# Kernel tuning notes

Measured on AMD Instinct MI355X. Metric: run time of the kernel, lower is better.

Reference implementation:

```python
import jax, jax.numpy as jnp
import numpy as np

E = 1024   # n_embd
H = 16     # n_heads
D = 64     # head_dim
G = 4      # n_kv_groups
F = 4096   # ffn hidden_dim
V = 32000  # vocab
L = 4      # n_layers (all full_attention)
B = 1
T = 2048
ROT = 16   # partial_rotary_factor 0.25 * head_dim 64, rounded to even
EPS = 1e-6
THETA = 10000.0


def rope_tables(seq_len):
    # matches compute_rope_params: inv_freq over even indices of rotary_dim
    inv_freq = 1.0 / (THETA ** (jnp.arange(0, ROT, 2, dtype=jnp.float32) / ROT))
    ang = jnp.arange(seq_len, dtype=jnp.float32)[:, None] * inv_freq[None, :]
    ang = jnp.concatenate([ang, ang], axis=1)  # [T, ROT]
    return jnp.cos(ang), jnp.sin(ang)


def rmsnorm(x, w):
    # torch RMSNorm: x * rsqrt(mean(x^2)+eps) * (1 + weight)
    xf = x.astype(jnp.float32)
    n = xf * jax.lax.rsqrt(jnp.mean(xf * xf, axis=-1, keepdims=True) + EPS)
    return (n * (1.0 + w)).astype(x.dtype)


def apply_rope(x, cos, sin):
    # x: [B, h, T, D]; cos/sin: [1, 1, T, ROT]; partial rotary on first ROT dims
    x_rot, x_pass = x[..., :ROT], x[..., ROT:]
    x1, x2 = x_rot[..., :ROT // 2], x_rot[..., ROT // 2:]
    rotated = jnp.concatenate([-x2, x1], axis=-1)
    return jnp.concatenate([x_rot * cos + rotated * sin, x_pass], axis=-1)


def _forward(tokens, emb, Wq, Wk, Wv, Wo, qn, kn, n1, n2, f1, f2, f3, fn, head):
    cos, sin = rope_tables(T)
    cos = cos[None, None]  # [1,1,T,ROT]
    sin = sin[None, None]
    mask = jnp.triu(jnp.ones((T, T), dtype=bool), k=1)  # True = masked
    scale = D ** -0.5
    x = emb[tokens]  # [B,T,E]

    def block(x, p):
        wq, wk, wv, wo, qw, kw, w1, w2, g1, g2, g3 = p
        h = rmsnorm(x, w1)
        # fused Q + gate projection -> [B,T,H,2D], chunk on last dim
        qg = (h @ wq).reshape(B, T, H, 2 * D)
        q = qg[..., :D].transpose(0, 2, 1, 3)            # [B,H,T,D]
        gate = qg[..., D:].reshape(B, T, H * D)          # [B,T,H*D]
        k = (h @ wk).reshape(B, T, G, D).transpose(0, 2, 1, 3)  # [B,G,T,D]
        v = (h @ wv).reshape(B, T, G, D).transpose(0, 2, 1, 3)
        q = rmsnorm(q, qw)
        k = rmsnorm(k, kw)
        q = apply_rope(q, cos, sin)
        k = apply_rope(k, cos, sin)
        k = jnp.repeat(k, H // G, axis=1)  # GQA expand -> [B,H,T,D]
        v = jnp.repeat(v, H // G, axis=1)
        scores = jnp.einsum('bhqd,bhkd->bhqk', q, k)
        scores = jnp.where(mask, -jnp.inf, scores) * scale
        w = jax.nn.softmax(scores.astype(jnp.float32), axis=-1).astype(q.dtype)
        ctx = jnp.einsum('bhqk,bhkd->bhqd', w, v)
        ctx = ctx.transpose(0, 2, 1, 3).reshape(B, T, H * D)
        ctx = ctx * jax.nn.sigmoid(gate)
        x = x + ctx @ wo
        h2 = rmsnorm(x, w2)
        ff = (jax.nn.silu(h2 @ g1) * (h2 @ g2)) @ g3
        return x + ff, None

    params = (Wq, Wk, Wv, Wo, qn, kn, n1, n2, f1, f2, f3)
    x, _ = jax.lax.scan(block, x, params)
    return rmsnorm(x, fn) @ head  # logits [B,T,V]


def setup_inputs() -> dict:
    key = jax.random.key(0)
    ks = jax.random.split(key, 16)
    s = 0.02
    rn = lambda k, shape, sc=s: jax.random.normal(k, shape, jnp.float32) * sc
    return {
        'tokens': jax.random.randint(ks[0], (B, T), 0, V),
        'emb': rn(ks[1], (V, E)),
        'Wq': rn(ks[2], (L, E, 2 * H * D)),
        'Wk': rn(ks[3], (L, E, G * D)),
        'Wv': rn(ks[4], (L, E, G * D)),
        'Wo': rn(ks[5], (L, H * D, E)),
        'qn': rn(ks[6], (L, D)),
        'kn': rn(ks[7], (L, D)),
        'n1': rn(ks[8], (L, E)),
        'n2': rn(ks[9], (L, E)),
        'f1': rn(ks[10], (L, E, F)),
        'f2': rn(ks[11], (L, E, F)),
        'f3': rn(ks[12], (L, F, E)),
        'fn': rn(ks[13], (E,)),
        'head': rn(ks[14], (E, V)),
    }


def reference(tokens, emb, Wq, Wk, Wv, Wo, qn, kn, n1, n2, f1, f2, f3, fn, head):
    return _forward(tokens, emb, Wq, Wk, Wv, Wo, qn, kn, n1, n2, f1, f2, f3, fn, head)
```

## Files before the change

kernel.cpp:

```cpp
#include <hip/hip_runtime.h>

#define T_LEN 2048
#define E_DIM 1024
#define H_N 16
#define G_N 4
#define D_H 64
#define F_DIM 4096
#define V_SZ 32000
#define L_N 4

typedef __attribute__((ext_vector_type(8))) __bf16 bf16x8;
typedef __attribute__((ext_vector_type(4))) float f32x4;

__device__ __forceinline__ unsigned short f2bf(float f){
  unsigned int u = __float_as_uint(f);
  unsigned int r = (u + 0x7FFFu + ((u >> 16) & 1u)) >> 16;
  return (unsigned short)r;
}

__device__ __forceinline__ unsigned int packbf(float a, float b){
  return (unsigned int)f2bf(a) | ((unsigned int)f2bf(b) << 16);
}

__device__ __forceinline__ f32x4 mfma16(bf16x8 a, bf16x8 b, f32x4 c){
  return __builtin_amdgcn_mfma_f32_16x16x32_bf16(a, b, c, 0, 0, 0);
}

__device__ __forceinline__ void gl16(const void* g, void* l){
  __builtin_amdgcn_global_load_lds((const __attribute__((address_space(1))) void*)g,
                                   (__attribute__((address_space(3))) void*)l, 16, 0, 0);
}

#define SBAR() __builtin_amdgcn_s_barrier()
#define LGK0() do{ asm volatile("s_waitcnt lgkmcnt(0)" ::: "memory"); __builtin_amdgcn_sched_barrier(0); }while(0)
#define VMC4() do{ asm volatile("s_waitcnt vmcnt(4)" ::: "memory"); __builtin_amdgcn_sched_barrier(0); }while(0)
#define VMC0() do{ asm volatile("s_waitcnt vmcnt(0)" ::: "memory"); __builtin_amdgcn_sched_barrier(0); }while(0)

#define QSCALE 0.1803368801111183f

__global__ __launch_bounds__(256) void embed_k(const float* __restrict__ emb,
                                               const int* __restrict__ tokens,
                                               float* __restrict__ x){
  int t = blockIdx.x;
  int tok = tokens[t];
  const float4* src = (const float4*)(emb + (size_t)tok * E_DIM);
  float4* dst = (float4*)(x + (size_t)t * E_DIM);
  dst[threadIdx.x] = src[threadIdx.x];
}

__global__ __launch_bounds__(256) void transpose_bf16(const float* __restrict__ src,
                                                      unsigned short* __restrict__ dst,
                                                      int R, int C){
  __shared__ float tile[32][33];
  int c0 = blockIdx.x * 32, r0 = blockIdx.y * 32;
  int tx = threadIdx.x & 31, ty = threadIdx.x >> 5;
  for (int i = 0; i < 4; i++){
    int r = ty + i * 8;
    tile[r][tx] = src[(size_t)(r0 + r) * C + c0 + tx];
  }
  __syncthreads();
  for (int i = 0; i < 4; i++){
    int r = ty + i * 8;
    dst[(size_t)(c0 + r) * R + r0 + tx] = f2bf(tile[tx][r]);
  }
}

__device__ __forceinline__ void tr32(const float* __restrict__ src, unsigned short* __restrict__ dst,
                                     int R, int C, int bx, int by, float* tile ){
  int c0 = bx * 32, r0 = by * 32;
  int tx = threadIdx.x & 31, ty = threadIdx.x >> 5;
  for (int i = 0; i < 4; i++){
    int r = ty + i * 8;
    tile[r * 33 + tx] = src[(size_t)(r0 + r) * C + c0 + tx];
  }
  __syncthreads();
  for (int i = 0; i < 4; i++){
    int r = ty + i * 8;
    dst[(size_t)(c0 + r) * R + r0 + tx] = f2bf(tile[tx * 33 + r]);
  }
}

__global__ __launch_bounds__(256) void prep_weights(const float* __restrict__ Wq, const float* __restrict__ Wk,
                                                    const float* __restrict__ Wv, const float* __restrict__ Wo,
                                                    const float* __restrict__ f1, const float* __restrict__ f2,
                                                    const float* __restrict__ f3,
                                                    unsigned short* __restrict__ wt_qkv,
                                                    unsigned short* __restrict__ wt_o,
                                                    unsigned short* __restrict__ wt_f12i,
                                                    unsigned short* __restrict__ wt_f3){
  __shared__ float sh[1100];
  int id = blockIdx.x;
  if (id < 2048){ tr32(Wq, wt_qkv, 1024, 2048, id & 63, id >> 6, sh); return; }
  id -= 2048;
  if (id < 256){ tr32(Wk, wt_qkv + 2048 * 1024, 1024, 256, id & 7, id >> 3, sh); return; }
  id -= 256;
  if (id < 256){ tr32(Wv, wt_qkv + 2304 * 1024, 1024, 256, id & 7, id >> 3, sh); return; }
  id -= 256;
  if (id < 1024){ tr32(Wo, wt_o, 1024, 1024, id & 31, id >> 5, sh); return; }
  id -= 1024;
  if (id < 4096){ tr32(f3, wt_f3, 4096, 1024, id & 31, id >> 5, sh); return; }
  id -= 4096;
  {
    int q = id & 255, kb = id >> 8;
    float* t1 = sh; float* t2 = sh + 32 * 17;
    int c = threadIdx.x & 15, kk0 = threadIdx.x >> 4;
    for (int p = 0; p < 2; p++){
      int kk = p * 16 + kk0;
      t1[kk * 17 + c] = f1[(size_t)(kb * 32 + kk) * F_DIM + q * 16 + c];
      t2[kk * 17 + c] = f2[(size_t)(kb * 32 + kk) * F_DIM + q * 16 + c];
    }
    __syncthreads();
    int kk = threadIdx.x & 31, rb = threadIdx.x >> 5;
    for (int i = 0; i < 4; i++){
      int r = i * 8 + rb;
      float v = (r < 16) ? t1[kk * 17 + r] : t2[kk * 17 + (r - 16)];
      wt_f12i[(size_t)(q * 32 + r) * 1024 + kb * 32 + kk] = f2bf(v);
    }
  }
}

__global__ __launch_bounds__(256) void rmsnorm_k(const float* __restrict__ x,
                                                 const float* __restrict__ w,
                                                 unsigned short* __restrict__ out){
  const int t = blockIdx.x, tid = threadIdx.x;
  const float4 v = ((const float4*)(x + (size_t)t * E_DIM))[tid];
  float ss = v.x*v.x + v.y*v.y + v.z*v.z + v.w*v.w;
  for (int m = 1; m < 64; m <<= 1) ss += __shfl_xor(ss, m);
  __shared__ float red[4];
  if ((tid & 63) == 0) red[tid >> 6] = ss;
  __syncthreads();
  ss = red[0] + red[1] + red[2] + red[3];
  const float r = rsqrtf(ss * (1.0f / E_DIM) + 1e-6f);
  const float4 wv = ((const float4*)w)[tid];
  ushort4 o;
  o.x = f2bf(v.x * r * (1.0f + wv.x));
  o.y = f2bf(v.y * r * (1.0f + wv.y));
  o.z = f2bf(v.z * r * (1.0f + wv.z));
  o.w = f2bf(v.w * r * (1.0f + wv.w));
  ((ushort4*)(out + (size_t)t * E_DIM))[tid] = o;
}

template<int MODE>
__global__ __launch_bounds__(512) void gemm128(const unsigned short* __restrict__ A,
                                               const unsigned short* __restrict__ Bt,
                                               float* __restrict__ C,
                                               int M, int N, int K){
  __shared__ unsigned short lds[49152];
  const int tid = threadIdx.x;
  const int lane = tid & 63, w = tid >> 6;
  const int wm = w >> 2, wn = w & 3;
  const int l15 = lane & 15, l4 = lane >> 4;

  const int nwg = gridDim.x;
  const int xcd = (int)blockIdx.x & 7, lin = (int)blockIdx.x >> 3;
  const int q8 = nwg >> 3, r8 = nwg & 7;
  const int wgid = (xcd < r8 ? xcd * (q8 + 1) : r8 * (q8 + 1) + (xcd - r8) * q8) + lin;
  const int nm = M >> 7;
  const int bm = wgid % nm, bn = wgid / nm;
  const int m0 = bm * 128, n0 = bn * 256;

  const int KS = K / gridDim.y;
  const int kbeg = blockIdx.y * KS;
  const int NT = KS >> 6;

  const int srow = (lane >> 3);
  const int scol = lane & 7;

  auto stageA = [&](int b, int kt){
    #pragma unroll
    for (int c = 0; c < 2; c++){
      int r = w * 16 + c * 8 + srow;
      const unsigned short* g = A + (size_t)(m0 + r) * K + kbeg + kt * 64 + ((scol ^ (r & 7)) << 3);
      gl16(g, (char*)lds + b * 16384 + (w * 16 + c * 8) * 128);
    }
  };
  auto stageB = [&](int b, int h, int kt){
    #pragma unroll
    for (int c = 0; c < 2; c++){
      int r = w * 16 + c * 8 + srow;
      const unsigned short* g = Bt + (size_t)(n0 + h * 128 + r) * K + kbeg + kt * 64 + ((scol ^ (r & 7)) << 3);
      gl16(g, (char*)lds + 32768 + (b * 2 + h) * 16384 + (w * 16 + c * 8) * 128);
    }
  };

  const int sl0 = ((l4)     ^ (l15 & 7)) << 4;
  const int sl1 = ((4 | l4) ^ (l15 & 7)) << 4;

  f32x4 acc[4][4] = {};
  bf16x8 aF[8], bF[8];

  stageA(0, 0); stageB(0, 0, 0); stageB(0, 1, 0);
  if (NT > 1){ stageB(1, 0, 1); stageB(1, 1, 1); }
  VMC4();
  SBAR();

  for (int kt = 0; kt < NT; kt++){
    const int buf = kt & 1;
    const char* Ab = (const char*)lds + buf * 16384;
    const char* Bb = (const char*)lds + 32768 + (buf * 2 + (wn >> 1)) * 16384;
    const int brbase = (wn & 1) * 64;

    #pragma unroll
    for (int mf = 0; mf < 4; mf++){
      int r = wm * 64 + mf * 16 + l15;
      aF[mf * 2 + 0] = *(const bf16x8*)(Ab + r * 128 + sl0);
      aF[mf * 2 + 1] = *(const bf16x8*)(Ab + r * 128 + sl1);
    }
    #pragma unroll
    for (int nf = 0; nf < 2; nf++){
      int r = brbase + nf * 16 + l15;
      bF[nf * 2 + 0] = *(const bf16x8*)(Bb + r * 128 + sl0);
      bF[nf * 2 + 1] = *(const bf16x8*)(Bb + r * 128 + sl1);
    }
    if (kt + 1 < NT) stageA(buf ^ 1, kt + 1);
    SBAR(); LGK0();
    __builtin_amdgcn_s_setprio(1);
    #pragma unroll
    for (int mf = 0; mf < 4; mf++)
      #pragma unroll
      for (int nf = 0; nf < 2; nf++){
        acc[mf][nf] = mfma16(aF[mf * 2 + 0], bF[nf * 2 + 0], acc[mf][nf]);
        acc[mf][nf] = mfma16(aF[mf * 2 + 1], bF[nf * 2 + 1], acc[mf][nf]);
      }
    __builtin_amdgcn_s_setprio(0);
    SBAR();

    #pragma unroll
    for (int nf = 2; nf < 4; nf++){
      int r = brbase + nf * 16 + l15;
      bF[nf * 2 + 0] = *(const bf16x8*)(Bb + r * 128 + sl0);
      bF[nf * 2 + 1] = *(const bf16x8*)(Bb + r * 128 + sl1);
    }
    SBAR(); LGK0();
    __builtin_amdgcn_s_setprio(1);
    #pragma unroll
    for (int mf = 0; mf < 4; mf++)
      #pragma unroll
      for (int nf = 2; nf < 4; nf++){
        acc[mf][nf] = mfma16(aF[mf * 2 + 0], bF[nf * 2 + 0], acc[mf][nf]);
        acc[mf][nf] = mfma16(aF[mf * 2 + 1], bF[nf * 2 + 1], acc[mf][nf]);
      }
    __builtin_amdgcn_s_setprio(0);
    SBAR();

    if (kt + 2 < NT){
      stageB(buf, 0, kt + 2);
      stageB(buf, 1, kt + 2);
      VMC4();
    } else {
      VMC0();
    }
    SBAR();
  }

  #pragma unroll
  for (int mf = 0; mf < 4; mf++)
    #pragma unroll
    for (int nf = 0; nf < 4; nf++){
      int col = n0 + wn * 64 + nf * 16 + l15;
      int row0 = m0 + wm * 64 + mf * 16 + l4 * 4;
      #pragma unroll
      for (int r = 0; r < 4; r++){
        size_t idx = (size_t)(row0 + r) * N + col;
        if (MODE == 0) C[idx] = acc[mf][nf][r];
        else atomicAdd(&C[idx], acc[mf][nf][r]);
      }
    }
}

template<int EPI>
__global__ __launch_bounds__(512, 2) void gemm256(const unsigned short* __restrict__ A,
                                                  const unsigned short* __restrict__ Bt,
                                                  float* __restrict__ outF,
                                                  unsigned short* __restrict__ outH,
                                                  int M, int N, int K){
  __shared__ unsigned short lds[65536];
  const int tid = threadIdx.x;
  const int lane = tid & 63, w = tid >> 6;
  const int wm = w >> 2, wn = w & 3;
  const int l15 = lane & 15, l4 = lane >> 4;

  const int nwg = gridDim.x;
  const int xcd = (int)blockIdx.x & 7, lin = (int)blockIdx.x >> 3;
  const int q8 = nwg >> 3, r8 = nwg & 7;
  const int wgid = (xcd < r8 ? xcd * (q8 + 1) : r8 * (q8 + 1) + (xcd - r8) * q8) + lin;
  const int nm = M >> 8;
  const int bm = wgid % nm, bn = wgid / nm;
  const int m0 = bm * 256, n0 = bn * 256;

  const int KS = K / gridDim.y;
  const int kbeg = blockIdx.y * KS;
  const int NT = KS >> 6;

  const int srow = (lane >> 3);
  const int scol = lane & 7;

  auto stageA = [&](int b, int h, int kt){
    #pragma unroll
    for (int c = 0; c < 2; c++){
      int r = w * 16 + c * 8 + srow;
      const unsigned short* g = A + (size_t)(m0 + h * 128 + r) * K + kbeg + kt * 64 + ((scol ^ (r & 7)) << 3);
      gl16(g, (char*)lds + (b * 2 + h) * 16384 + (w * 16 + c * 8) * 128);
    }
  };
  auto stageB = [&](int b, int h, int kt){
    #pragma unroll
    for (int c = 0; c < 2; c++){
      int r = w * 16 + c * 8 + srow;
      const unsigned short* g = Bt + (size_t)(n0 + h * 128 + r) * K + kbeg + kt * 64 + ((scol ^ (r & 7)) << 3);
      gl16(g, (char*)lds + 65536 + (b * 2 + h) * 16384 + (w * 16 + c * 8) * 128);
    }
  };

  const int sl0 = ((l4)     ^ (l15 & 7)) << 4;
  const int sl1 = ((4 | l4) ^ (l15 & 7)) << 4;

  f32x4 acc[8][4] = {};
  bf16x8 aF[8], bF[8];

  stageA(0, 0, 0); stageA(0, 1, 0); stageB(0, 0, 0); stageB(0, 1, 0);
  if (NT > 1){ stageB(1, 0, 1); stageB(1, 1, 1); }
  VMC4();
  SBAR();

  for (int kt = 0; kt < NT; kt++){
    const int buf = kt & 1;
    const char* Ab = (const char*)lds + (buf * 2 + wm) * 16384;
    const char* Bb = (const char*)lds + 65536 + (buf * 2 + (wn >> 1)) * 16384;
    const int brbase = (wn & 1) * 64;

    #pragma unroll
    for (int mf = 0; mf < 4; mf++){
      int r = mf * 16 + l15;
      aF[mf * 2 + 0] = *(const bf16x8*)(Ab + r * 128 + sl0);
      aF[mf * 2 + 1] = *(const bf16x8*)(Ab + r * 128 + sl1);
    }
    #pragma unroll
    for (int nf = 0; nf < 2; nf++){
      int r = brbase + nf * 16 + l15;
      bF[nf * 2 + 0] = *(const bf16x8*)(Bb + r * 128 + sl0);
      bF[nf * 2 + 1] = *(const bf16x8*)(Bb + r * 128 + sl1);
    }
    if (kt + 1 < NT) stageA(buf ^ 1, 0, kt + 1);
    SBAR(); LGK0();
    __builtin_amdgcn_s_setprio(1);
    #pragma unroll
    for (int mf = 0; mf < 4; mf++)
      #pragma unroll
      for (int nf = 0; nf < 2; nf++){
        acc[mf][nf] = mfma16(aF[mf * 2 + 0], bF[nf * 2 + 0], acc[mf][nf]);
        acc[mf][nf] = mfma16(aF[mf * 2 + 1], bF[nf * 2 + 1], acc[mf][nf]);
      }
    __builtin_amdgcn_s_setprio(0);
    SBAR();

    #pragma unroll
    for (int nf = 2; nf < 4; nf++){
      int r = brbase + nf * 16 + l15;
      bF[nf * 2 + 0] = *(const bf16x8*)(Bb + r * 128 + sl0);
      bF[nf * 2 + 1] = *(const bf16x8*)(Bb + r * 128 + sl1);
    }
    if (kt + 1 < NT) stageA(buf ^ 1, 1, kt + 1);
    SBAR(); LGK0();
    __builtin_amdgcn_s_setprio(1);
    #pragma unroll
    for (int mf = 0; mf < 4; mf++)
      #pragma unroll
      for (int nf = 2; nf < 4; nf++){
        acc[mf][nf] = mfma16(aF[mf * 2 + 0], bF[nf * 2 + 0], acc[mf][nf]);
        acc[mf][nf] = mfma16(aF[mf * 2 + 1], bF[nf * 2 + 1], acc[mf][nf]);
      }
    __builtin_amdgcn_s_setprio(0);
    SBAR();

    #pragma unroll
    for (int mf = 0; mf < 4; mf++){
      int r = 64 + mf * 16 + l15;
      aF[mf * 2 + 0] = *(const bf16x8*)(Ab + r * 128 + sl0);
      aF[mf * 2 + 1] = *(const bf16x8*)(Ab + r * 128 + sl1);
    }
    if (kt + 2 < NT) stageB(buf, 0, kt + 2);
    SBAR(); LGK0();
    __builtin_amdgcn_s_setprio(1);
    #pragma unroll
    for (int mf = 0; mf < 4; mf++)
      #pragma unroll
      for (int nf = 2; nf < 4; nf++){
        acc[4 + mf][nf] = mfma16(aF[mf * 2 + 0], bF[nf * 2 + 0], acc[4 + mf][nf]);
        acc[4 + mf][nf] = mfma16(aF[mf * 2 + 1], bF[nf * 2 + 1], acc[4 + mf][nf]);
      }
    __builtin_amdgcn_s_setprio(0);
    SBAR();

    if (kt + 2 < NT) stageB(buf, 1, kt + 2);
    SBAR();
    __builtin_amdgcn_s_setprio(1);
    #pragma unroll
    for (int mf = 0; mf < 4; mf++)
      #pragma unroll
      for (int nf = 0; nf < 2; nf++){
        acc[4 + mf][nf] = mfma16(aF[mf * 2 + 0], bF[nf * 2 + 0], acc[4 + mf][nf]);
        acc[4 + mf][nf] = mfma16(aF[mf * 2 + 1], bF[nf * 2 + 1], acc[4 + mf][nf]);
      }
    __builtin_amdgcn_s_setprio(0);
    if (kt + 2 < NT) { VMC4(); } else { VMC0(); }
    SBAR();
  }

  if (EPI == 0 || EPI == 2){
    #pragma unroll
    for (int mfg = 0; mfg < 8; mfg++){
      #pragma unroll
      for (int nf = 0; nf < 4; nf++){
        int col = n0 + wn * 64 + nf * 16 + l15;
        int row0 = m0 + wm * 128 + mfg * 16 + l4 * 4;
        #pragma unroll
        for (int r = 0; r < 4; r++){
          size_t idx = (size_t)(row0 + r) * N + col;
          if (EPI == 0) outF[idx] = acc[mfg][nf][r];
          else atomicAdd(&outF[idx], acc[mfg][nf][r]);
        }
      }
    }
  } else {
    const int NH = N >> 1;
    #pragma unroll
    for (int mfg = 0; mfg < 8; mfg++){
      #pragma unroll
      for (int nfp = 0; nfp < 2; nfp++){
        int col = (n0 >> 1) + wn * 32 + nfp * 16 + l15;
        int row0 = m0 + wm * 128 + mfg * 16 + l4 * 4;
        #pragma unroll
        for (int r = 0; r < 4; r++){
          float u = acc[mfg][nfp * 2 + 0][r];
          float g = acc[mfg][nfp * 2 + 1][r];
          outH[(size_t)(row0 + r) * NH + col] = f2bf(u / (1.0f + __expf(-u)) * g);
        }
      }
    }
  }
}

__global__ __launch_bounds__(256) void qkvpost_k(const float* __restrict__ qkv,
                                                 const float* __restrict__ qn,
                                                 const float* __restrict__ kn,
                                                 unsigned short* __restrict__ qb,
                                                 unsigned short* __restrict__ kb,
                                                 unsigned short* __restrict__ vt){
  const int t = blockIdx.x;
  const int lane = threadIdx.x & 63, w = threadIdx.x >> 6;
  const int d = lane;
  const int fi = d & 7;
  const float invf = powf(10000.0f, -(float)fi * 0.125f);
  const float ang = (float)t * invf;
  const float c = cosf(ang), s = sinf(ang);

  for (int i = 0; i < 4; i++){
    int h = w * 4 + i;
    float v = qkv[(size_t)t * 2560 + h * 128 + d];
    float ss = v * v;
    for (int m = 1; m < 64; m <<= 1) ss += __shfl_xor(ss, m);
    float r = rsqrtf(ss * (1.0f / D_H) + 1e-6f);
    float xn = v * r * (1.0f + qn[d]);
    float partner = __shfl_xor(xn, 8);
    float o;
    if (d < 8)       o = xn * c - partner * s;
    else if (d < 16) o = xn * c + partner * s;
    else             o = xn;
    qb[((size_t)h * T_LEN + t) * D_H + d] = f2bf(o * QSCALE);
  }
  {
    float v = qkv[(size_t)t * 2560 + 2048 + w * 64 + d];
    float ss = v * v;
    for (int m = 1; m < 64; m <<= 1) ss += __shfl_xor(ss, m);
    float r = rsqrtf(ss * (1.0f / D_H) + 1e-6f);
    float xn = v * r * (1.0f + kn[d]);
    float partner = __shfl_xor(xn, 8);
    float o;
    if (d < 8)       o = xn * c - partner * s;
    else if (d < 16) o = xn * c + partner * s;
    else             o = xn;
    kb[((size_t)w * T_LEN + t) * D_H + d] = f2bf(o);
  }
  {
    float v = qkv[(size_t)t * 2560 + 2304 + w * 64 + d];
    vt[((size_t)(w * 64 + d)) * T_LEN + t] = f2bf(v);
  }
}

__global__ __launch_bounds__(256) void attn_k(const unsigned short* __restrict__ qb,
                                              const unsigned short* __restrict__ kb,
                                              const unsigned short* __restrict__ vt,
                                              const float* __restrict__ qkv,
                                              unsigned short* __restrict__ ctxg){
  const int qt = blockIdx.x, h = blockIdx.y;
  const int g = h >> 2;
  const int tid = threadIdx.x;
  const int wv = tid >> 6;
  const int lane = tid & 63;
  const int l15 = lane & 15, l4 = lane >> 4;
  const int q0 = qt * 16;
  const int nch = (q0 >> 6) + 1;

  __shared__ unsigned short Pl[4][16][72];
  __shared__ float sO[4][16][66];
  __shared__ float sM[4][16];
  __shared__ float sL[4][16];

  const bf16x8 aq0 = *(const bf16x8*)(qb + ((size_t)h * T_LEN + q0 + l15) * D_H + l4 * 8);
  const bf16x8 aq1 = *(const bf16x8*)(qb + ((size_t)h * T_LEN + q0 + l15) * D_H + 32 + l4 * 8);

  f32x4 acc[4] = {};
  float m = -1e30f, lpart = 0.0f;

  for (int c = wv; c < nch; c += 4){
    const int kv0 = c << 6;
    f32x4 sc[4];
    #pragma unroll
    for (int cp = 0; cp < 4; cp++){
      const unsigned short* kbase = kb + ((size_t)g * T_LEN + kv0 + cp * 16 + l15) * D_H + l4 * 8;
      bf16x8 bk0 = *(const bf16x8*)(kbase);
      bf16x8 bk1 = *(const bf16x8*)(kbase + 32);
      f32x4 z = {0.f, 0.f, 0.f, 0.f};
      z = mfma16(bk0, aq0, z);
      z = mfma16(bk1, aq1, z);
      sc[cp] = z;
    }
    if (c == nch - 1){
      #pragma unroll
      for (int cp = 0; cp < 4; cp++)
        #pragma unroll
        for (int j = 0; j < 4; j++){
          int kv = kv0 + cp * 16 + l4 * 4 + j;
          sc[cp][j] = (kv <= q0 + l15) ? sc[cp][j] : -1e30f;
        }
    }
    float mx = sc[0][0];
    #pragma unroll
    for (int cp = 0; cp < 4; cp++)
      #pragma unroll
      for (int j = 0; j < 4; j++) mx = fmaxf(mx, sc[cp][j]);
    mx = fmaxf(mx, __shfl_xor(mx, 16));
    mx = fmaxf(mx, __shfl_xor(mx, 32));
    const float mnew = fmaxf(m, mx);
    const bool grew = !__all(mnew == m);
    const float mold = m;
    m = mnew;

    float ssum = 0.0f;
    unsigned int up[4][2];
    #pragma unroll
    for (int cp = 0; cp < 4; cp++){
      float p0 = exp2f(sc[cp][0] - mnew);
      float p1 = exp2f(sc[cp][1] - mnew);
      float p2 = exp2f(sc[cp][2] - mnew);
      float p3 = exp2f(sc[cp][3] - mnew);
      ssum += (p0 + p1) + (p2 + p3);
      up[cp][0] = packbf(p0, p1);
      up[cp][1] = packbf(p2, p3);
    }
    if (grew){
      const float resc = exp2f(mold - mnew);
      lpart *= resc;
      float r0 = __shfl(resc, l4 * 4 + 0);
      float r1 = __shfl(resc, l4 * 4 + 1);
      float r2 = __shfl(resc, l4 * 4 + 2);
      float r3 = __shfl(resc, l4 * 4 + 3);
      #pragma unroll
      for (int nt = 0; nt < 4; nt++){
        acc[nt][0] *= r0; acc[nt][1] *= r1; acc[nt][2] *= r2; acc[nt][3] *= r3;
      }
    }
    lpart += ssum;

    #pragma unroll
    for (int cp = 0; cp < 4; cp++){
      uint2 pr; pr.x = up[cp][0]; pr.y = up[cp][1];
      *(uint2*)&Pl[wv][l15][cp * 16 + l4 * 4] = pr;
    }
    asm volatile("s_waitcnt lgkmcnt(0)" ::: "memory");
    const bf16x8 pa0 = *(const bf16x8*)&Pl[wv][l15][l4 * 8];
    const bf16x8 pa1 = *(const bf16x8*)&Pl[wv][l15][32 + l4 * 8];
    #pragma unroll
    for (int nt = 0; nt < 4; nt++){
      const unsigned short* vbase = vt + ((size_t)g * 64 + nt * 16 + l15) * T_LEN + kv0;
      bf16x8 bv0 = *(const bf16x8*)(vbase + l4 * 8);
      bf16x8 bv1 = *(const bf16x8*)(vbase + 32 + l4 * 8);
      acc[nt] = mfma16(pa1, bv1, mfma16(pa0, bv0, acc[nt]));
    }
  }

  lpart += __shfl_xor(lpart, 16);
  lpart += __shfl_xor(lpart, 32);

  #pragma unroll
  for (int j = 0; j < 4; j++){
    int row = l4 * 4 + j;
    #pragma unroll
    for (int nt = 0; nt < 4; nt++)
      sO[wv][row][nt * 16 + l15] = acc[nt][j];
  }
  if (l4 == 0){
    sM[wv][l15] = m;
    sL[wv][l15] = lpart;
  }
  __syncthreads();

  #pragma unroll
  for (int rr = 0; rr < 4; rr++){
    int r = wv * 4 + rr;
    float m0 = sM[0][r], m1 = sM[1][r], m2 = sM[2][r], m3 = sM[3][r];
    float ms = fmaxf(fmaxf(m0, m1), fmaxf(m2, m3));
    float w0 = exp2f(m0 - ms), w1 = exp2f(m1 - ms), w2 = exp2f(m2 - ms), w3 = exp2f(m3 - ms);
    float accv = w0 * sO[0][r][lane] + w1 * sO[1][r][lane] + w2 * sO[2][r][lane] + w3 * sO[3][r][lane];
    float lsum = w0 * sL[0][r] + w1 * sL[1][r] + w2 * sL[2][r] + w3 * sL[3][r];
    float gate = qkv[(size_t)(q0 + r) * 2560 + h * 128 + 64 + lane];
    float val = accv / lsum * (1.0f / (1.0f + __expf(-gate)));
    ctxg[(size_t)(q0 + r) * (H_N * D_H) + h * D_H + lane] = f2bf(val);
  }
}

extern "C" void kernel_launch(void* const* d_in, const int* in_sizes, int n_in,
                              void* d_out, int out_size, void* d_ws, size_t ws_size,
                              hipStream_t stream){
  (void)in_sizes; (void)n_in; (void)out_size; (void)ws_size;
  const int*   tokens = (const int*)d_in[0];
  const float* emb    = (const float*)d_in[1];
  const float* Wq     = (const float*)d_in[2];
  const float* Wk     = (const float*)d_in[3];
  const float* Wv     = (const float*)d_in[4];
  const float* Wo     = (const float*)d_in[5];
  const float* qn     = (const float*)d_in[6];
  const float* kn     = (const float*)d_in[7];
  const float* n1     = (const float*)d_in[8];
  const float* n2     = (const float*)d_in[9];
  const float* f1     = (const float*)d_in[10];
  const float* f2     = (const float*)d_in[11];
  const float* f3     = (const float*)d_in[12];
  const float* fn     = (const float*)d_in[13];
  const float* head   = (const float*)d_in[14];
  float* out = (float*)d_out;

  char* ws = (char*)d_ws;
  size_t off = 0;
  auto alloc = [&](size_t bytes)->char*{
    char* p = ws + off;
    off += (bytes + 255) & ~(size_t)255;
    return p;
  };
  float*          x       = (float*)alloc((size_t)T_LEN * E_DIM * 4);
  unsigned short* hbf     = (unsigned short*)alloc((size_t)T_LEN * E_DIM * 2);
  float*          qkvf    = (float*)alloc((size_t)T_LEN * 2560 * 4);
  unsigned short* qb      = (unsigned short*)alloc((size_t)H_N * T_LEN * D_H * 2);
  unsigned short* kb      = (unsigned short*)alloc((size_t)G_N * T_LEN * D_H * 2);
  unsigned short* vt      = (unsigned short*)alloc((size_t)G_N * D_H * T_LEN * 2);
  unsigned short* ctxg    = (unsigned short*)alloc((size_t)T_LEN * E_DIM * 2);
  unsigned short* hg      = (unsigned short*)alloc((size_t)T_LEN * F_DIM * 2);
  unsigned short* wt_qkv  = (unsigned short*)alloc((size_t)2560 * E_DIM * 2);
  unsigned short* wt_o    = (unsigned short*)alloc((size_t)E_DIM * E_DIM * 2);
  unsigned short* wt_f12i = (unsigned short*)alloc((size_t)2 * F_DIM * E_DIM * 2);
  unsigned short* wt_f3   = (unsigned short*)alloc((size_t)E_DIM * F_DIM * 2);
  unsigned short* wt_head = (unsigned short*)alloc((size_t)V_SZ * E_DIM * 2);

  embed_k<<<T_LEN, 256, 0, stream>>>(emb, tokens, x);
  transpose_bf16<<<dim3(V_SZ / 32, E_DIM / 32), 256, 0, stream>>>(head, wt_head, E_DIM, V_SZ);

  for (int l = 0; l < L_N; l++){
    prep_weights<<<15872, 256, 0, stream>>>(Wq + (size_t)l * E_DIM * 2048,
                                            Wk + (size_t)l * E_DIM * 256,
                                            Wv + (size_t)l * E_DIM * 256,
                                            Wo + (size_t)l * E_DIM * E_DIM,
                                            f1 + (size_t)l * E_DIM * F_DIM,
                                            f2 + (size_t)l * E_DIM * F_DIM,
                                            f3 + (size_t)l * F_DIM * E_DIM,
                                            wt_qkv, wt_o, wt_f12i, wt_f3);

    rmsnorm_k<<<T_LEN, 256, 0, stream>>>(x, n1 + l * E_DIM, hbf);
    gemm128<0><<<(T_LEN / 128) * (2560 / 256), 512, 0, stream>>>(hbf, wt_qkv, qkvf, T_LEN, 2560, E_DIM);
    qkvpost_k<<<T_LEN, 256, 0, stream>>>(qkvf, qn + l * D_H, kn + l * D_H, qb, kb, vt);
    attn_k<<<dim3(T_LEN / 16, H_N), 256, 0, stream>>>(qb, kb, vt, qkvf, ctxg);
    gemm128<2><<<dim3((T_LEN / 128) * (E_DIM / 256), 4), 512, 0, stream>>>(ctxg, wt_o, x, T_LEN, E_DIM, E_DIM);

    rmsnorm_k<<<T_LEN, 256, 0, stream>>>(x, n2 + l * E_DIM, hbf);
    gemm256<1><<<(T_LEN / 256) * (2 * F_DIM / 256), 512, 0, stream>>>(hbf, wt_f12i, nullptr, hg, T_LEN, 2 * F_DIM, E_DIM);
    gemm256<2><<<dim3((T_LEN / 256) * (E_DIM / 256), 8), 512, 0, stream>>>(hg, wt_f3, x, nullptr, T_LEN, E_DIM, F_DIM);
  }

  rmsnorm_k<<<T_LEN, 256, 0, stream>>>(x, fn, hbf);
  gemm256<0><<<(T_LEN / 256) * (V_SZ / 256), 512, 0, stream>>>(hbf, wt_head, out, nullptr, T_LEN, V_SZ, E_DIM);
}
```

Before: 1.396 ms.

## Fuse QK-norm, RoPE and gate sigmoid into QKV GEMM epilogue; batch weight prep

Moves the per-head RMSNorm, partial RoPE, Q scaling, K/V layout conversion and gate sigmoid into the QKV GEMM epilogue. This removes the fp32 qkv intermediate and the separate qkvpost kernel, and attention now reads the gate as a precomputed bf16 sigmoid. Weight transposition for all layers is also launched once, ahead of the layer loop, into per-layer buffers. The cost is a larger workspace, more epilogue register pressure with cos/sin computed per element, and scattered stores for the V transpose.

```diff
diff --git a/kernel.cpp b/kernel.cpp
--- a/kernel.cpp
+++ b/kernel.cpp
@@ -16,6 +16,10 @@
   unsigned int u = __float_as_uint(f);
   unsigned int r = (u + 0x7FFFu + ((u >> 16) & 1u)) >> 16;
   return (unsigned short)r;
+}
+
+__device__ __forceinline__ float bf2f(unsigned short u){
+  return __uint_as_float((unsigned int)u << 16);
 }
 
 __device__ __forceinline__ unsigned int packbf(float a, float b){
@@ -80,16 +84,32 @@
   }
 }
 
-__global__ __launch_bounds__(256) void prep_weights(const float* __restrict__ Wq, const float* __restrict__ Wk,
-                                                    const float* __restrict__ Wv, const float* __restrict__ Wo,
-                                                    const float* __restrict__ f1, const float* __restrict__ f2,
-                                                    const float* __restrict__ f3,
-                                                    unsigned short* __restrict__ wt_qkv,
-                                                    unsigned short* __restrict__ wt_o,
-                                                    unsigned short* __restrict__ wt_f12i,
-                                                    unsigned short* __restrict__ wt_f3){
+#define PREP_PER_LAYER 15872
+
+__global__ __launch_bounds__(256) void prep_weights(const float* __restrict__ Wq_, const float* __restrict__ Wk_,
+                                                    const float* __restrict__ Wv_, const float* __restrict__ Wo_,
+                                                    const float* __restrict__ f1_, const float* __restrict__ f2_,
+                                                    const float* __restrict__ f3_,
+                                                    unsigned short* __restrict__ wt_qkv_,
+                                                    unsigned short* __restrict__ wt_o_,
+                                                    unsigned short* __restrict__ wt_f12i_,
+                                                    unsigned short* __restrict__ wt_f3_){
   __shared__ float sh[1100];
   int id = blockIdx.x;
+  const int l = id / PREP_PER_LAYER;
+  id -= l * PREP_PER_LAYER;
+  const float* Wq = Wq_ + (size_t)l * E_DIM * 2048;
+  const float* Wk = Wk_ + (size_t)l * E_DIM * 256;
+  const float* Wv = Wv_ + (size_t)l * E_DIM * 256;
+  const float* Wo = Wo_ + (size_t)l * E_DIM * E_DIM;
+  const float* f1 = f1_ + (size_t)l * E_DIM * F_DIM;
+  const float* f2 = f2_ + (size_t)l * E_DIM * F_DIM;
+  const float* f3 = f3_ + (size_t)l * F_DIM * E_DIM;
+  unsigned short* wt_qkv  = wt_qkv_  + (size_t)l * 2560 * E_DIM;
+  unsigned short* wt_o    = wt_o_    + (size_t)l * E_DIM * E_DIM;
+  unsigned short* wt_f12i = wt_f12i_ + (size_t)l * 2 * F_DIM * E_DIM;
+  unsigned short* wt_f3   = wt_f3_   + (size_t)l * E_DIM * F_DIM;
+
   if (id < 2048){ tr32(Wq, wt_qkv, 1024, 2048, id & 63, id >> 6, sh); return; }
   id -= 2048;
   if (id < 256){ tr32(Wk, wt_qkv + 2048 * 1024, 1024, 256, id & 7, id >> 3, sh); return; }
@@ -144,7 +164,13 @@
 __global__ __launch_bounds__(512) void gemm128(const unsigned short* __restrict__ A,
                                                const unsigned short* __restrict__ Bt,
                                                float* __restrict__ C,
-                                               int M, int N, int K){
+                                               int M, int N, int K,
+                                               const float* __restrict__ qn,
+                                               const float* __restrict__ kn,
+                                               unsigned short* __restrict__ qb,
+                                               unsigned short* __restrict__ kb,
+                                               unsigned short* __restrict__ vtb,
+                                               unsigned short* __restrict__ sg){
   __shared__ unsigned short lds[49152];
   const int tid = threadIdx.x;
   const int lane = tid & 63, w = tid >> 6;
@@ -253,19 +279,106 @@
     SBAR();
   }
 
-  #pragma unroll
-  for (int mf = 0; mf < 4; mf++)
-    #pragma unroll
-    for (int nf = 0; nf < 4; nf++){
-      int col = n0 + wn * 64 + nf * 16 + l15;
-      int row0 = m0 + wm * 64 + mf * 16 + l4 * 4;
-      #pragma unroll
-      for (int r = 0; r < 4; r++){
-        size_t idx = (size_t)(row0 + r) * N + col;
-        if (MODE == 0) C[idx] = acc[mf][nf][r];
-        else atomicAdd(&C[idx], acc[mf][nf][r]);
-      }
-    }
+  if (MODE == 0 || MODE == 2){
+    #pragma unroll
+    for (int mf = 0; mf < 4; mf++)
+      #pragma unroll
+      for (int nf = 0; nf < 4; nf++){
+        int col = n0 + wn * 64 + nf * 16 + l15;
+        int row0 = m0 + wm * 64 + mf * 16 + l4 * 4;
+        #pragma unroll
+        for (int r = 0; r < 4; r++){
+          size_t idx = (size_t)(row0 + r) * N + col;
+          if (MODE == 0) C[idx] = acc[mf][nf][r];
+          else atomicAdd(&C[idx], acc[mf][nf][r]);
+        }
+      }
+  } else {
+    const int cbase = n0 + wn * 64;
+    if (cbase < 2048){
+      const int h = cbase >> 7;
+      if ((cbase & 64) == 0){
+        const float qw0 = qn[l15], qw1 = qn[16 + l15], qw2 = qn[32 + l15], qw3 = qn[48 + l15];
+        const float invf = powf(10000.0f, -(float)(l15 & 7) * 0.125f);
+        #pragma unroll
+        for (int mf = 0; mf < 4; mf++)
+          #pragma unroll
+          for (int r = 0; r < 4; r++){
+            float ss = 0.0f;
+            #pragma unroll
+            for (int nf = 0; nf < 4; nf++) ss += acc[mf][nf][r] * acc[mf][nf][r];
+            ss += __shfl_xor(ss, 1); ss += __shfl_xor(ss, 2);
+            ss += __shfl_xor(ss, 4); ss += __shfl_xor(ss, 8);
+            const float rs = rsqrtf(ss * (1.0f / 64.0f) + 1e-6f);
+            const int t = m0 + wm * 64 + mf * 16 + l4 * 4 + r;
+            const float ang = (float)t * invf;
+            const float cc = cosf(ang), sn = sinf(ang);
+            float x0 = acc[mf][0][r] * rs * (1.0f + qw0);
+            float x1 = acc[mf][1][r] * rs * (1.0f + qw1);
+            float x2 = acc[mf][2][r] * rs * (1.0f + qw2);
+            float x3 = acc[mf][3][r] * rs * (1.0f + qw3);
+            float partner = __shfl_xor(x0, 8);
+            float o0 = (l15 < 8) ? (x0 * cc - partner * sn) : (x0 * cc + partner * sn);
+            unsigned short* qrow = qb + ((size_t)h * T_LEN + t) * 64;
+            qrow[l15]      = f2bf(o0 * QSCALE);
+            qrow[16 + l15] = f2bf(x1 * QSCALE);
+            qrow[32 + l15] = f2bf(x2 * QSCALE);
+            qrow[48 + l15] = f2bf(x3 * QSCALE);
+          }
+      } else {
+        #pragma unroll
+        for (int mf = 0; mf < 4; mf++)
+          #pragma unroll
+          for (int r = 0; r < 4; r++){
+            const int t = m0 + wm * 64 + mf * 16 + l4 * 4 + r;
+            unsigned short* srow = sg + (size_t)t * 1024 + h * 64;
+            #pragma unroll
+            for (int nf = 0; nf < 4; nf++)
+              srow[nf * 16 + l15] = f2bf(1.0f / (1.0f + __expf(-acc[mf][nf][r])));
+          }
+      }
+    } else if (cbase < 2304){
+      const int g = (cbase - 2048) >> 6;
+      const float kw0 = kn[l15], kw1 = kn[16 + l15], kw2 = kn[32 + l15], kw3 = kn[48 + l15];
+      const float invf = powf(10000.0f, -(float)(l15 & 7) * 0.125f);
+      #pragma unroll
+      for (int mf = 0; mf < 4; mf++)
+        #pragma unroll
+        for (int r = 0; r < 4; r++){
+          float ss = 0.0f;
+          #pragma unroll
+          for (int nf = 0; nf < 4; nf++) ss += acc[mf][nf][r] * acc[mf][nf][r];
+          ss += __shfl_xor(ss, 1); ss += __shfl_xor(ss, 2);
+          ss += __shfl_xor(ss, 4); ss += __shfl_xor(ss, 8);
+          const float rs = rsqrtf(ss * (1.0f / 64.0f) + 1e-6f);
+          const int t = m0 + wm * 64 + mf * 16 + l4 * 4 + r;
+          const float ang = (float)t * invf;
+          const float cc = cosf(ang), sn = sinf(ang);
+          float x0 = acc[mf][0][r] * rs * (1.0f + kw0);
+          float x1 = acc[mf][1][r] * rs * (1.0f + kw1);
+          float x2 = acc[mf][2][r] * rs * (1.0f + kw2);
+          float x3 = acc[mf][3][r] * rs * (1.0f + kw3);
+          float partner = __shfl_xor(x0, 8);
+          float o0 = (l15 < 8) ? (x0 * cc - partner * sn) : (x0 * cc + partner * sn);
+          unsigned short* krow = kb + ((size_t)g * T_LEN + t) * 64;
+          krow[l15]      = f2bf(o0);
+          krow[16 + l15] = f2bf(x1);
+          krow[32 + l15] = f2bf(x2);
+          krow[48 + l15] = f2bf(x3);
+        }
+    } else {
+      const int g = (cbase - 2304) >> 6;
+      #pragma unroll
+      for (int mf = 0; mf < 4; mf++)
+        #pragma unroll
+        for (int r = 0; r < 4; r++){
+          const int t = m0 + wm * 64 + mf * 16 + l4 * 4 + r;
+          #pragma unroll
+          for (int nf = 0; nf < 4; nf++)
+            vtb[((size_t)g * 64 + nf * 16 + l15) * T_LEN + t] = f2bf(acc[mf][nf][r]);
+        }
+    }
+  }
 }
 
 template<int EPI>
@@ -441,57 +554,10 @@
   }
 }
 
-__global__ __launch_bounds__(256) void qkvpost_k(const float* __restrict__ qkv,
-                                                 const float* __restrict__ qn,
-                                                 const float* __restrict__ kn,
-                                                 unsigned short* __restrict__ qb,
-                                                 unsigned short* __restrict__ kb,
-                                                 unsigned short* __restrict__ vt){
-  const int t = blockIdx.x;
-  const int lane = threadIdx.x & 63, w = threadIdx.x >> 6;
-  const int d = lane;
-  const int fi = d & 7;
-  const float invf = powf(10000.0f, -(float)fi * 0.125f);
-  const float ang = (float)t * invf;
-  const float c = cosf(ang), s = sinf(ang);
-
-  for (int i = 0; i < 4; i++){
-    int h = w * 4 + i;
-    float v = qkv[(size_t)t * 2560 + h * 128 + d];
-    float ss = v * v;
-    for (int m = 1; m < 64; m <<= 1) ss += __shfl_xor(ss, m);
-    float r = rsqrtf(ss * (1.0f / D_H) + 1e-6f);
-    float xn = v * r * (1.0f + qn[d]);
-    float partner = __shfl_xor(xn, 8);
-    float o;
-    if (d < 8)       o = xn * c - partner * s;
-    else if (d < 16) o = xn * c + partner * s;
-    else             o = xn;
-    qb[((size_t)h * T_LEN + t) * D_H + d] = f2bf(o * QSCALE);
-  }
-  {
-    float v = qkv[(size_t)t * 2560 + 2048 + w * 64 + d];
-    float ss = v * v;
-    for (int m = 1; m < 64; m <<= 1) ss += __shfl_xor(ss, m);
-    float r = rsqrtf(ss * (1.0f / D_H) + 1e-6f);
-    float xn = v * r * (1.0f + kn[d]);
-    float partner = __shfl_xor(xn, 8);
-    float o;
-    if (d < 8)       o = xn * c - partner * s;
-    else if (d < 16) o = xn * c + partner * s;
-    else             o = xn;
-    kb[((size_t)w * T_LEN + t) * D_H + d] = f2bf(o);
-  }
-  {
-    float v = qkv[(size_t)t * 2560 + 2304 + w * 64 + d];
-    vt[((size_t)(w * 64 + d)) * T_LEN + t] = f2bf(v);
-  }
-}
-
 __global__ __launch_bounds__(256) void attn_k(const unsigned short* __restrict__ qb,
                                               const unsigned short* __restrict__ kb,
                                               const unsigned short* __restrict__ vt,
-                                              const float* __restrict__ qkv,
+                                              const unsigned short* __restrict__ sgate,
                                               unsigned short* __restrict__ ctxg){
   const int qt = blockIdx.x, h = blockIdx.y;
   const int g = h >> 2;
@@ -614,8 +680,8 @@
     float w0 = exp2f(m0 - ms), w1 = exp2f(m1 - ms), w2 = exp2f(m2 - ms), w3 = exp2f(m3 - ms);
     float accv = w0 * sO[0][r][lane] + w1 * sO[1][r][lane] + w2 * sO[2][r][lane] + w3 * sO[3][r][lane];
     float lsum = w0 * sL[0][r] + w1 * sL[1][r] + w2 * sL[2][r] + w3 * sL[3][r];
-    float gate = qkv[(size_t)(q0 + r) * 2560 + h * 128 + 64 + lane];
-    float val = accv / lsum * (1.0f / (1.0f + __expf(-gate)));
+    float sgv = bf2f(sgate[(size_t)(q0 + r) * 1024 + h * 64 + lane]);
+    float val = accv / lsum * sgv;
     ctxg[(size_t)(q0 + r) * (H_N * D_H) + h * D_H + lane] = f2bf(val);
   }
 }
@@ -648,38 +714,37 @@
     off += (bytes + 255) & ~(size_t)255;
     return p;
   };
-  float*          x       = (float*)alloc((size_t)T_LEN * E_DIM * 4);
-  unsigned short* hbf     = (unsigned short*)alloc((size_t)T_LEN * E_DIM * 2);
-  float*          qkvf    = (float*)alloc((size_t)T_LEN * 2560 * 4);
-  unsigned short* qb      = (unsigned short*)alloc((size_t)H_N * T_LEN * D_H * 2);
-  unsigned short* kb      = (unsigned short*)alloc((size_t)G_N * T_LEN * D_H * 2);
-  unsigned short* vt      = (unsigned short*)alloc((size_t)G_N * D_H * T_LEN * 2);
-  unsigned short* ctxg    = (unsigned short*)alloc((size_t)T_LEN * E_DIM * 2);
-  unsigned short* hg      = (unsigned short*)alloc((size_t)T_LEN * F_DIM * 2);
-  unsigned short* wt_qkv  = (unsigned short*)alloc((size_t)2560 * E_DIM * 2);
-  unsigned short* wt_o    = (unsigned short*)alloc((size_t)E_DIM * E_DIM * 2);
-  unsigned short* wt_f12i = (unsigned short*)alloc((size_t)2 * F_DIM * E_DIM * 2);
-  unsigned short* wt_f3   = (unsigned short*)alloc((size_t)E_DIM * F_DIM * 2);
-  unsigned short* wt_head = (unsigned short*)alloc((size_t)V_SZ * E_DIM * 2);
+  float*          x        = (float*)alloc((size_t)T_LEN * E_DIM * 4);
+  unsigned short* hbf      = (unsigned short*)alloc((size_t)T_LEN * E_DIM * 2);
+  unsigned short* qb       = (unsigned short*)alloc((size_t)H_N * T_LEN * D_H * 2);
+  unsigned short* kb       = (unsigned short*)alloc((size_t)G_N * T_LEN * D_H * 2);
+  unsigned short* vt       = (unsigned short*)alloc((size_t)G_N * D_H * T_LEN * 2);
+  unsigned short* sgate    = (unsigned short*)alloc((size_t)T_LEN * E_DIM * 2);
+  unsigned short* ctxg     = (unsigned short*)alloc((size_t)T_LEN * E_DIM * 2);
+  unsigned short* hg       = (unsigned short*)alloc((size_t)T_LEN * F_DIM * 2);
+  unsigned short* wt_qkv4  = (unsigned short*)alloc((size_t)L_N * 2560 * E_DIM * 2);
+  unsigned short* wt_o4    = (unsigned short*)alloc((size_t)L_N * E_DIM * E_DIM * 2);
+  unsigned short* wt_f12i4 = (unsigned short*)alloc((size_t)L_N * 2 * F_DIM * E_DIM * 2);
+  unsigned short* wt_f34   = (unsigned short*)alloc((size_t)L_N * E_DIM * F_DIM * 2);
+  unsigned short* wt_head  = (unsigned short*)alloc((size_t)V_SZ * E_DIM * 2);
 
   embed_k<<<T_LEN, 256, 0, stream>>>(emb, tokens, x);
   transpose_bf16<<<dim3(V_SZ / 32, E_DIM / 32), 256, 0, stream>>>(head, wt_head, E_DIM, V_SZ);
+  prep_weights<<<L_N * PREP_PER_LAYER, 256, 0, stream>>>(Wq, Wk, Wv, Wo, f1, f2, f3,
+                                                         wt_qkv4, wt_o4, wt_f12i4, wt_f34);
 
   for (int l = 0; l < L_N; l++){
-    prep_weights<<<15872, 256, 0, stream>>>(Wq + (size_t)l * E_DIM * 2048,
-                                            Wk + (size_t)l * E_DIM * 256,
-                                            Wv + (size_t)l * E_DIM * 256,
-                                            Wo + (size_t)l * E_DIM * E_DIM,
-                                            f1 + (size_t)l * E_DIM * F_DIM,
-                                            f2 + (size_t)l * E_DIM * F_DIM,
-                                            f3 + (size_t)l * F_DIM * E_DIM,
-                                            wt_qkv, wt_o, wt_f12i, wt_f3);
+    const unsigned short* wt_qkv  = wt_qkv4  + (size_t)l * 2560 * E_DIM;
+    const unsigned short* wt_o    = wt_o4    + (size_t)l * E_DIM * E_DIM;
+    const unsigned short* wt_f12i = wt_f12i4 + (size_t)l * 2 * F_DIM * E_DIM;
+    const unsigned short* wt_f3   = wt_f34   + (size_t)l * E_DIM * F_DIM;
 
     rmsnorm_k<<<T_LEN, 256, 0, stream>>>(x, n1 + l * E_DIM, hbf);
-    gemm128<0><<<(T_LEN / 128) * (2560 / 256), 512, 0, stream>>>(hbf, wt_qkv, qkvf, T_LEN, 2560, E_DIM);
-    qkvpost_k<<<T_LEN, 256, 0, stream>>>(qkvf, qn + l * D_H, kn + l * D_H, qb, kb, vt);
-    attn_k<<<dim3(T_LEN / 16, H_N), 256, 0, stream>>>(qb, kb, vt, qkvf, ctxg);
-    gemm128<2><<<dim3((T_LEN / 128) * (E_DIM / 256), 4), 512, 0, stream>>>(ctxg, wt_o, x, T_LEN, E_DIM, E_DIM);
+    gemm128<3><<<(T_LEN / 128) * (2560 / 256), 512, 0, stream>>>(hbf, wt_qkv, nullptr, T_LEN, 2560, E_DIM,
+                                                                 qn + l * D_H, kn + l * D_H, qb, kb, vt, sgate);
+    attn_k<<<dim3(T_LEN / 16, H_N), 256, 0, stream>>>(qb, kb, vt, sgate, ctxg);
+    gemm128<2><<<dim3((T_LEN / 128) * (E_DIM / 256), 4), 512, 0, stream>>>(ctxg, wt_o, x, T_LEN, E_DIM, E_DIM,
+                                                                           nullptr, nullptr, nullptr, nullptr, nullptr, nullptr);
 
     rmsnorm_k<<<T_LEN, 256, 0, stream>>>(x, n2 + l * E_DIM, hbf);
     gemm256<1><<<(T_LEN / 256) * (2 * F_DIM / 256), 512, 0, stream>>>(hbf, wt_f12i, nullptr, hg, T_LEN, 2 * F_DIM, E_DIM);
```

Result: no change. 1.401 ms (+0.4%).
